# Kernel optimization log

Hardware: AMD Instinct MI355X
Metric: run time of the kernel (lower is better)

## Reference

```python
import jax, jax.numpy as jnp
import numpy as np

DIM = 1024
HEADS = 16
HEAD_DIM = DIM // HEADS
SCALE = HEAD_DIM ** -0.5


def setup_inputs() -> dict:
    key = jax.random.key(0)
    ks = jax.random.split(key, 9)
    B, S, D = 2, 2048, DIM
    std = 1.0 / np.sqrt(D)
    Z = jax.random.normal(ks[0], (B, S, D), dtype=jnp.float32)
    Wq = jax.random.uniform(ks[1], (D, D), jnp.float32, -std, std)
    bq = jax.random.uniform(ks[2], (D,), jnp.float32, -std, std)
    Wk = jax.random.uniform(ks[3], (D, D), jnp.float32, -std, std)
    bk = jax.random.uniform(ks[4], (D,), jnp.float32, -std, std)
    Wv = jax.random.uniform(ks[5], (D, D), jnp.float32, -std, std)
    bv = jax.random.uniform(ks[6], (D,), jnp.float32, -std, std)
    Wo = jax.random.uniform(ks[7], (D, D), jnp.float32, -std, std)
    bo = jax.random.uniform(ks[8], (D,), jnp.float32, -std, std)
    return {"Z": Z, "Wq": Wq, "bq": bq, "Wk": Wk, "bk": bk,
            "Wv": Wv, "bv": bv, "Wo": Wo, "bo": bo}


def reference(Z, Wq, bq, Wk, bk, Wv, bv, Wo, bo):
    B, S, D = Z.shape
    H, Hd = HEADS, HEAD_DIM
    # torch Linear: y = x @ W.T + b
    Q = (Z @ Wq.T + bq).reshape(B, S, H, Hd).transpose(0, 2, 1, 3)  # [B,H,S,Hd]
    K = (Z @ Wk.T + bk).reshape(B, S, H, Hd).transpose(0, 2, 1, 3)
    V = (Z @ Wv.T + bv).reshape(B, S, H, Hd).transpose(0, 2, 1, 3)
    scores = jnp.einsum('bhqd,bhkd->bhqk', Q, K) * SCALE  # [B,H,S,S]
    weights = jax.nn.softmax(scores, axis=-1)
    weights = jnp.nan_to_num(weights, nan=0.0)
    # dropout=0.0 -> identity (eval mode)
    out = jnp.einsum('bhqk,bhkd->bhqd', weights, V)  # [B,H,S,Hd]
    out = out.transpose(0, 2, 1, 3).reshape(B, S, D)
    return out @ Wo.T + bo
```

## Files before the change

kernel.cpp:

```cpp
#include <hip/hip_runtime.h>
#include <hip/hip_bf16.h>
#include <stdint.h>

typedef unsigned short u16;
typedef __bf16 bf16x8 __attribute__((ext_vector_type(8)));
typedef float f32x4 __attribute__((ext_vector_type(4)));
typedef float f32x16 __attribute__((ext_vector_type(16)));

#define D_MODEL 1024
#define SEQ     2048
#define NB      2
#define NH      16
#define HD      64
#define M_TOT   (NB*SEQ)
#define ATT_SCALE 0.125f

__device__ __forceinline__ u16 f2bf(float f) {
  union { __bf16 b; u16 u; } cv; cv.b = (__bf16)f; return cv.u;
}

__device__ __forceinline__ void async_copy16(void* lds_dst, const void* gsrc) {
  __builtin_amdgcn_global_load_lds(
      (const __attribute__((address_space(1))) unsigned int*)gsrc,
      (__attribute__((address_space(3))) unsigned int*)lds_dst, 16, 0, 0);
}

__global__ void cvt_all(const float* __restrict__ Z,  const float* __restrict__ Wq,
                        const float* __restrict__ Wk, const float* __restrict__ Wv,
                        const float* __restrict__ Wo,
                        u16* __restrict__ Zb,  u16* __restrict__ Wqb,
                        u16* __restrict__ Wkb, u16* __restrict__ Wvb,
                        u16* __restrict__ Wob)
{
  int i = blockIdx.x * 256 + threadIdx.x;
  const float* src; u16* dst; int off;
  if (i < (1 << 20)) { src = Z; dst = Zb; off = i; }
  else {
    int j = i - (1 << 20);
    int seg = j >> 18; off = j & ((1 << 18) - 1);
    src = (seg == 0) ? Wq : (seg == 1) ? Wk : (seg == 2) ? Wv : Wo;
    dst = (seg == 0) ? Wqb : (seg == 1) ? Wkb : (seg == 2) ? Wvb : Wob;
  }
  float4 v = reinterpret_cast<const float4*>(src)[off];
  ushort4 o;
  o.x = f2bf(v.x); o.y = f2bf(v.y); o.z = f2bf(v.z); o.w = f2bf(v.w);
  reinterpret_cast<ushort4*>(dst)[off] = o;
}

template<int F32OUT, int TRANSV>
__global__ __launch_bounds__(256, 3)
void gemm_bt(const u16* __restrict__ A,
             const u16* __restrict__ B0, const u16* __restrict__ B1, const u16* __restrict__ B2,
             const float* __restrict__ bias0, const float* __restrict__ bias1, const float* __restrict__ bias2,
             void* __restrict__ C0, void* __restrict__ C1, void* __restrict__ C2,
             float s0, float s1, float s2,
             int M, int N, int K)
{
  (void)M;
  const int z = blockIdx.z;
  const u16* Bt = (z == 0) ? B0 : ((z == 1) ? B1 : B2);
  const float* bias = (z == 0) ? bias0 : ((z == 1) ? bias1 : bias2);
  void* Cout = (z == 0) ? C0 : ((z == 1) ? C1 : C2);
  const float oscl = (z == 0) ? s0 : ((z == 1) ? s1 : s2);

  __shared__ u16 lds_a[2][128*32];
  __shared__ u16 lds_b[2][128*32];

  const int tid = threadIdx.x;
  const int w = tid >> 6, lane = tid & 63;
  const int l15 = lane & 15, lhi = lane >> 4;
  const int m0 = blockIdx.y * 128, n0 = blockIdx.x * 128;
  const int wm = w >> 1, wn = w & 1;

  f32x4 acc[4][4] = {};

  auto stage = [&](int buf, int kt) {
    const int k0 = kt * 32;
    #pragma unroll
    for (int i = 0; i < 2; ++i) {
      const int base = (w*2 + i) * 1024;
      const int pos  = base + (lane << 4);
      const int row  = pos >> 6;
      const int slot = (pos >> 4) & 3;
      const int ss   = slot ^ ((row >> 1) & 3);
      async_copy16((char*)lds_a[buf] + base,
                   (const char*)(A  + (size_t)(m0 + row) * K + k0 + ss*8));
      async_copy16((char*)lds_b[buf] + base,
                   (const char*)(Bt + (size_t)(n0 + row) * K + k0 + ss*8));
    }
  };

  auto compute = [&](int buf) {
    bf16x8 af[4], bf[4];
    #pragma unroll
    for (int mi = 0; mi < 4; ++mi) {
      const int row = wm*64 + mi*16 + l15;
      const int s   = lhi ^ ((row >> 1) & 3);
      af[mi] = *reinterpret_cast<const bf16x8*>((const char*)lds_a[buf] + row*64 + s*16);
    }
    #pragma unroll
    for (int ni = 0; ni < 4; ++ni) {
      const int row = wn*64 + ni*16 + l15;
      const int s   = lhi ^ ((row >> 1) & 3);
      bf[ni] = *reinterpret_cast<const bf16x8*>((const char*)lds_b[buf] + row*64 + s*16);
    }
    #pragma unroll
    for (int mi = 0; mi < 4; ++mi)
      #pragma unroll
      for (int ni = 0; ni < 4; ++ni)
        acc[mi][ni] = __builtin_amdgcn_mfma_f32_16x16x32_bf16(af[mi], bf[ni], acc[mi][ni], 0, 0, 0);
  };

  stage(0, 0);
  __syncthreads();
  const int nk = K >> 5;
  for (int kt = 0; kt < nk; ++kt) {
    if (kt + 1 < nk) stage((kt + 1) & 1, kt + 1);
    compute(kt & 1);
    __syncthreads();
  }

  #pragma unroll
  for (int mi = 0; mi < 4; ++mi) {
    const int rowb = m0 + wm*64 + mi*16 + (lhi << 2);
    #pragma unroll
    for (int ni = 0; ni < 4; ++ni) {
      const int col = n0 + wn*64 + ni*16 + l15;
      const float bb = bias[col];
      if (TRANSV && z == 2) {
        ushort4 o4;
        o4.x = f2bf(acc[mi][ni][0] + bb);
        o4.y = f2bf(acc[mi][ni][1] + bb);
        o4.z = f2bf(acc[mi][ni][2] + bb);
        o4.w = f2bf(acc[mi][ni][3] + bb);
        const int bb2 = rowb >> 11, s = rowb & (SEQ - 1);
        const int hh = col >> 6, dd = col & 63;
        *reinterpret_cast<ushort4*>((u16*)Cout + ((size_t)(bb2*NH + hh)*HD + dd)*SEQ + s) = o4;
      } else {
        #pragma unroll
        for (int r = 0; r < 4; ++r) {
          const float v = (acc[mi][ni][r] + bb) * oscl;
          if (F32OUT)
            reinterpret_cast<float*>(Cout)[(size_t)(rowb + r) * N + col] = v;
          else
            reinterpret_cast<u16*>(Cout)[(size_t)(rowb + r) * N + col] = f2bf(v);
        }
      }
    }
  }
}

__global__ __launch_bounds__(256, 2)
void attn32(const u16* __restrict__ Qb, const u16* __restrict__ Kb,
            const u16* __restrict__ Vt, u16* __restrict__ Ob)
{
  __shared__ u16 vt[2][64*64];

  const int tid = threadIdx.x;
  const int w = tid >> 6, lane = tid & 63;
  const int l31 = lane & 31, hi = lane >> 5;
  const int bh = blockIdx.y, b = bh >> 4, h = bh & 15;
  const int qrow = blockIdx.x * 128 + w * 32 + l31;

  bf16x8 qf[4];
  {
    const u16* qp = Qb + (size_t)(b*SEQ + qrow) * D_MODEL + h*HD + hi*8;
    #pragma unroll
    for (int kc = 0; kc < 4; ++kc)
      qf[kc] = *reinterpret_cast<const bf16x8*>(qp + kc*16);
  }

  const u16* Vtg = Vt + (size_t)bh * HD * SEQ;

  float mrun = -1e30f, lrun = 0.f;
  f32x16 o0 = {}, o1 = {};

  auto stageV = [&](int buf, int kv0) {
    #pragma unroll
    for (int i = 0; i < 2; ++i) {
      const int c = i*256 + tid;
      const int d = c >> 3;
      const int sl = c & 7;
      const int sg = sl ^ (d & 7);
      async_copy16((char*)vt[buf] + (size_t)(i*256 + w*64)*16,
                   (const char*)(Vtg + (size_t)d*SEQ + kv0 + sg*8));
    }
  };

  stageV(0, 0);
  __syncthreads();
  int buf = 0;

  for (int kv0 = 0; kv0 < SEQ; kv0 += 64) {
    if (kv0 + 64 < SEQ) stageV(buf ^ 1, kv0 + 64);

    f32x16 s0 = {}, s1 = {};
    {
      const u16* kp = Kb + (size_t)(b*SEQ + kv0 + l31) * D_MODEL + h*HD + hi*8;
      #pragma unroll
      for (int kc = 0; kc < 4; ++kc) {
        bf16x8 ka = *reinterpret_cast<const bf16x8*>(kp + kc*16);
        s0 = __builtin_amdgcn_mfma_f32_32x32x16_bf16(ka, qf[kc], s0, 0, 0, 0);
      }
      const u16* kp1 = kp + (size_t)32 * D_MODEL;
      #pragma unroll
      for (int kc = 0; kc < 4; ++kc) {
        bf16x8 ka = *reinterpret_cast<const bf16x8*>(kp1 + kc*16);
        s1 = __builtin_amdgcn_mfma_f32_32x32x16_bf16(ka, qf[kc], s1, 0, 0, 0);
      }
    }

    float tmax = s0[0];
    #pragma unroll
    for (int r = 1; r < 16; ++r) tmax = fmaxf(tmax, s0[r]);
    #pragma unroll
    for (int r = 0; r < 16; ++r) tmax = fmaxf(tmax, s1[r]);
    tmax = fmaxf(tmax, __shfl_xor(tmax, 32));
    const float mnew = fmaxf(mrun, tmax);
    float rs = 0.f;
    #pragma unroll
    for (int r = 0; r < 16; ++r) { s0[r] = __expf(s0[r] - mnew); rs += s0[r]; }
    #pragma unroll
    for (int r = 0; r < 16; ++r) { s1[r] = __expf(s1[r] - mnew); rs += s1[r]; }
    rs += __shfl_xor(rs, 32);
    const float a = __expf(mrun - mnew);
    lrun = lrun * a + rs;
    mrun = mnew;
    #pragma unroll
    for (int r = 0; r < 16; ++r) { o0[r] *= a; o1[r] *= a; }

    unsigned pwA[2][8];
    #pragma unroll
    for (int a4 = 0; a4 < 4; ++a4)
      #pragma unroll
      for (int zz = 0; zz < 2; ++zz) {
        pwA[0][a4*2+zz] = (unsigned)f2bf(s0[4*a4+2*zz]) | ((unsigned)f2bf(s0[4*a4+2*zz+1]) << 16);
        pwA[1][a4*2+zz] = (unsigned)f2bf(s1[4*a4+2*zz]) | ((unsigned)f2bf(s1[4*a4+2*zz+1]) << 16);
      }

    const char* vb = (const char*)vt[buf];
    #pragma unroll
    for (int ks = 0; ks < 4; ++ks) {
      const int kb = ks >> 1, sm = ks & 1;
      unsigned keep0 = hi ? pwA[kb][(2*sm+1)*2+0] : pwA[kb][(2*sm)*2+0];
      unsigned keep1 = hi ? pwA[kb][(2*sm+1)*2+1] : pwA[kb][(2*sm)*2+1];
      unsigned send0 = hi ? pwA[kb][(2*sm)*2+0]   : pwA[kb][(2*sm+1)*2+0];
      unsigned send1 = hi ? pwA[kb][(2*sm)*2+1]   : pwA[kb][(2*sm+1)*2+1];
      unsigned recv0 = (unsigned)__shfl_xor((int)send0, 32);
      unsigned recv1 = (unsigned)__shfl_xor((int)send1, 32);
      union { bf16x8 f; unsigned u[4]; } pf;
      pf.u[0] = hi ? recv0 : keep0;
      pf.u[1] = hi ? recv1 : keep1;
      pf.u[2] = hi ? keep0 : recv0;
      pf.u[3] = hi ? keep1 : recv1;

      const int slg = ks*2 + hi;
      const int sw  = slg ^ (l31 & 7);
      bf16x8 va0 = *reinterpret_cast<const bf16x8*>(vb + (size_t)(l31*8 + sw)*16);
      bf16x8 va1 = *reinterpret_cast<const bf16x8*>(vb + (size_t)((l31+32)*8 + sw)*16);

      o0 = __builtin_amdgcn_mfma_f32_32x32x16_bf16(va0, pf.f, o0, 0, 0, 0);
      o1 = __builtin_amdgcn_mfma_f32_32x32x16_bf16(va1, pf.f, o1, 0, 0, 0);
    }

    __syncthreads();
    buf ^= 1;
  }

  const float inv = 1.0f / lrun;
  u16* op = Ob + (size_t)(b*SEQ + qrow) * D_MODEL + h*HD;
  #pragma unroll
  for (int a4 = 0; a4 < 4; ++a4) {
    ushort4 v0, v1;
    v0.x = f2bf(o0[4*a4+0]*inv); v0.y = f2bf(o0[4*a4+1]*inv);
    v0.z = f2bf(o0[4*a4+2]*inv); v0.w = f2bf(o0[4*a4+3]*inv);
    v1.x = f2bf(o1[4*a4+0]*inv); v1.y = f2bf(o1[4*a4+1]*inv);
    v1.z = f2bf(o1[4*a4+2]*inv); v1.w = f2bf(o1[4*a4+3]*inv);
    *reinterpret_cast<ushort4*>(op + 8*a4 + 4*hi)      = v0;
    *reinterpret_cast<ushort4*>(op + 32 + 8*a4 + 4*hi) = v1;
  }
}

extern "C" void kernel_launch(void* const* d_in, const int* in_sizes, int n_in,
                              void* d_out, int out_size, void* d_ws, size_t ws_size,
                              hipStream_t stream)
{
  (void)in_sizes; (void)n_in; (void)out_size;
  const float* Z  = (const float*)d_in[0];
  const float* Wq = (const float*)d_in[1];
  const float* bq = (const float*)d_in[2];
  const float* Wk = (const float*)d_in[3];
  const float* bk = (const float*)d_in[4];
  const float* Wv = (const float*)d_in[5];
  const float* bv = (const float*)d_in[6];
  const float* Wo = (const float*)d_in[7];
  const float* bo = (const float*)d_in[8];
  float* out = (float*)d_out;

  const size_t needed = (size_t)(M_TOT*D_MODEL)*2*5 + (size_t)(D_MODEL*D_MODEL)*2*4;
  if (ws_size < needed) return;

  u16* Zb  = (u16*)d_ws;
  u16* Wqb = Zb  + (size_t)M_TOT*D_MODEL;
  u16* Wkb = Wqb + (size_t)D_MODEL*D_MODEL;
  u16* Wvb = Wkb + (size_t)D_MODEL*D_MODEL;
  u16* Wob = Wvb + (size_t)D_MODEL*D_MODEL;
  u16* Qb  = Wob + (size_t)D_MODEL*D_MODEL;
  u16* Kb  = Qb  + (size_t)M_TOT*D_MODEL;
  u16* Vt  = Kb  + (size_t)M_TOT*D_MODEL;
  u16* Ab  = Vt  + (size_t)M_TOT*D_MODEL;

  cvt_all<<<dim3(8192), 256, 0, stream>>>(Z, Wq, Wk, Wv, Wo, Zb, Wqb, Wkb, Wvb, Wob);

  dim3 gproj(D_MODEL/128, M_TOT/128, 3);
  gemm_bt<0,1><<<gproj, 256, 0, stream>>>(Zb, Wqb, Wkb, Wvb, bq, bk, bv,
                                          (void*)Qb, (void*)Kb, (void*)Vt,
                                          ATT_SCALE, 1.0f, 1.0f,
                                          M_TOT, D_MODEL, D_MODEL);

  dim3 gattn(SEQ/128, NB*NH);
  attn32<<<gattn, 256, 0, stream>>>(Qb, Kb, Vt, Ab);

  dim3 gout(D_MODEL/128, M_TOT/128, 1);
  gemm_bt<1,0><<<gout, 256, 0, stream>>>(Ab, Wob, Wob, Wob, bo, bo, bo,
                                         (void*)out, (void*)out, (void*)out,
                                         1.0f, 1.0f, 1.0f,
                                         M_TOT, D_MODEL, D_MODEL);
}
```

Before: 240.6 us.

## Stage K tiles in LDS, use exp2 softmax with deferred rescale, swap V MFMA

K tiles are now loaded into swizzled LDS double buffers with async copies alongside V, replacing per-lane strided global loads inside the attention loop. The log2(e) factor is folded into the Q scale so softmax uses the hardware exp2, and the running-max rescale is skipped unless some lane's new max exceeds the old one by more than a threshold. In the V projection, the MFMA operands are swapped so the transposed V layout comes straight out of the accumulator. The trade-offs are more LDS per block and unrescaled exponent values that can grow up to 2^8 before a rescale, which costs some numerical headroom.

```diff
diff --git a/kernel.cpp b/kernel.cpp
--- a/kernel.cpp
+++ b/kernel.cpp
@@ -13,10 +13,14 @@
 #define NH      16
 #define HD      64
 #define M_TOT   (NB*SEQ)
-#define ATT_SCALE 0.125f
+#define QSCALE  (0.125f * 1.44269504088896f)
+#define DEFER_THR 8.0f
 
 __device__ __forceinline__ u16 f2bf(float f) {
   union { __bf16 b; u16 u; } cv; cv.b = (__bf16)f; return cv.u;
+}
+__device__ __forceinline__ float exp2_fast(float x) {
+  return __builtin_amdgcn_exp2f(x);
 }
 
 __device__ __forceinline__ void async_copy16(void* lds_dst, const void* gsrc) {
@@ -62,6 +66,7 @@
   const float* bias = (z == 0) ? bias0 : ((z == 1) ? bias1 : bias2);
   void* Cout = (z == 0) ? C0 : ((z == 1) ? C1 : C2);
   const float oscl = (z == 0) ? s0 : ((z == 1) ? s1 : s2);
+  const bool vswap = TRANSV && (z == 2);
 
   __shared__ u16 lds_a[2][128*32];
   __shared__ u16 lds_b[2][128*32];
@@ -104,11 +109,19 @@
       const int s   = lhi ^ ((row >> 1) & 3);
       bf[ni] = *reinterpret_cast<const bf16x8*>((const char*)lds_b[buf] + row*64 + s*16);
     }
-    #pragma unroll
-    for (int mi = 0; mi < 4; ++mi)
-      #pragma unroll
-      for (int ni = 0; ni < 4; ++ni)
-        acc[mi][ni] = __builtin_amdgcn_mfma_f32_16x16x32_bf16(af[mi], bf[ni], acc[mi][ni], 0, 0, 0);
+    if (vswap) {
+      #pragma unroll
+      for (int mi = 0; mi < 4; ++mi)
+        #pragma unroll
+        for (int ni = 0; ni < 4; ++ni)
+          acc[mi][ni] = __builtin_amdgcn_mfma_f32_16x16x32_bf16(bf[ni], af[mi], acc[mi][ni], 0, 0, 0);
+    } else {
+      #pragma unroll
+      for (int mi = 0; mi < 4; ++mi)
+        #pragma unroll
+        for (int ni = 0; ni < 4; ++ni)
+          acc[mi][ni] = __builtin_amdgcn_mfma_f32_16x16x32_bf16(af[mi], bf[ni], acc[mi][ni], 0, 0, 0);
+    }
   };
 
   stage(0, 0);
@@ -120,23 +133,30 @@
     __syncthreads();
   }
 
-  #pragma unroll
-  for (int mi = 0; mi < 4; ++mi) {
-    const int rowb = m0 + wm*64 + mi*16 + (lhi << 2);
-    #pragma unroll
-    for (int ni = 0; ni < 4; ++ni) {
-      const int col = n0 + wn*64 + ni*16 + l15;
-      const float bb = bias[col];
-      if (TRANSV && z == 2) {
-        ushort4 o4;
-        o4.x = f2bf(acc[mi][ni][0] + bb);
-        o4.y = f2bf(acc[mi][ni][1] + bb);
-        o4.z = f2bf(acc[mi][ni][2] + bb);
-        o4.w = f2bf(acc[mi][ni][3] + bb);
-        const int bb2 = rowb >> 11, s = rowb & (SEQ - 1);
-        const int hh = col >> 6, dd = col & 63;
-        *reinterpret_cast<ushort4*>((u16*)Cout + ((size_t)(bb2*NH + hh)*HD + dd)*SEQ + s) = o4;
-      } else {
+  if (vswap) {
+    #pragma unroll
+    for (int mi = 0; mi < 4; ++mi) {
+      const int sglob = m0 + wm*64 + mi*16 + l15;
+      const int b2 = sglob >> 11, s = sglob & (SEQ - 1);
+      #pragma unroll
+      for (int ni = 0; ni < 4; ++ni) {
+        #pragma unroll
+        for (int r = 0; r < 4; ++r) {
+          const int dglob = n0 + wn*64 + ni*16 + (lhi << 2) + r;
+          const int hh = dglob >> 6, dd = dglob & 63;
+          const float v = acc[mi][ni][r] + bias[dglob];
+          reinterpret_cast<u16*>(Cout)[((size_t)(b2*NH + hh)*HD + dd)*SEQ + s] = f2bf(v);
+        }
+      }
+    }
+  } else {
+    #pragma unroll
+    for (int mi = 0; mi < 4; ++mi) {
+      const int rowb = m0 + wm*64 + mi*16 + (lhi << 2);
+      #pragma unroll
+      for (int ni = 0; ni < 4; ++ni) {
+        const int col = n0 + wn*64 + ni*16 + l15;
+        const float bb = bias[col];
         #pragma unroll
         for (int r = 0; r < 4; ++r) {
           const float v = (acc[mi][ni][r] + bb) * oscl;
@@ -155,6 +175,7 @@
             const u16* __restrict__ Vt, u16* __restrict__ Ob)
 {
   __shared__ u16 vt[2][64*64];
+  __shared__ u16 kt[2][64*64];
 
   const int tid = threadIdx.x;
   const int w = tid >> 6, lane = tid & 63;
@@ -171,11 +192,12 @@
   }
 
   const u16* Vtg = Vt + (size_t)bh * HD * SEQ;
+  const u16* Kg  = Kb + (size_t)(b*SEQ) * D_MODEL + h*HD;
 
   float mrun = -1e30f, lrun = 0.f;
   f32x16 o0 = {}, o1 = {};
 
-  auto stageV = [&](int buf, int kv0) {
+  auto stageKV = [&](int buf, int kv0) {
     #pragma unroll
     for (int i = 0; i < 2; ++i) {
       const int c = i*256 + tid;
@@ -185,28 +207,34 @@
       async_copy16((char*)vt[buf] + (size_t)(i*256 + w*64)*16,
                    (const char*)(Vtg + (size_t)d*SEQ + kv0 + sg*8));
     }
+    #pragma unroll
+    for (int i = 0; i < 2; ++i) {
+      const int c = i*256 + tid;
+      const int key = c >> 3;
+      const int sl = c & 7;
+      const int sg = sl ^ (key & 7);
+      async_copy16((char*)kt[buf] + (size_t)(i*256 + w*64)*16,
+                   (const char*)(Kg + (size_t)(kv0 + key)*D_MODEL + sg*8));
+    }
   };
 
-  stageV(0, 0);
+  stageKV(0, 0);
   __syncthreads();
   int buf = 0;
 
   for (int kv0 = 0; kv0 < SEQ; kv0 += 64) {
-    if (kv0 + 64 < SEQ) stageV(buf ^ 1, kv0 + 64);
+    if (kv0 + 64 < SEQ) stageKV(buf ^ 1, kv0 + 64);
 
     f32x16 s0 = {}, s1 = {};
     {
-      const u16* kp = Kb + (size_t)(b*SEQ + kv0 + l31) * D_MODEL + h*HD + hi*8;
+      const char* kbp = (const char*)kt[buf];
       #pragma unroll
       for (int kc = 0; kc < 4; ++kc) {
-        bf16x8 ka = *reinterpret_cast<const bf16x8*>(kp + kc*16);
-        s0 = __builtin_amdgcn_mfma_f32_32x32x16_bf16(ka, qf[kc], s0, 0, 0, 0);
-      }
-      const u16* kp1 = kp + (size_t)32 * D_MODEL;
-      #pragma unroll
-      for (int kc = 0; kc < 4; ++kc) {
-        bf16x8 ka = *reinterpret_cast<const bf16x8*>(kp1 + kc*16);
-        s1 = __builtin_amdgcn_mfma_f32_32x32x16_bf16(ka, qf[kc], s1, 0, 0, 0);
+        const int sw = (kc*2 + hi) ^ (l31 & 7);
+        bf16x8 ka0 = *reinterpret_cast<const bf16x8*>(kbp + (size_t)(l31*8 + sw)*16);
+        s0 = __builtin_amdgcn_mfma_f32_32x32x16_bf16(ka0, qf[kc], s0, 0, 0, 0);
+        bf16x8 ka1 = *reinterpret_cast<const bf16x8*>(kbp + (size_t)((l31+32)*8 + sw)*16);
+        s1 = __builtin_amdgcn_mfma_f32_32x32x16_bf16(ka1, qf[kc], s1, 0, 0, 0);
       }
     }
 
@@ -216,18 +244,21 @@
     #pragma unroll
     for (int r = 0; r < 16; ++r) tmax = fmaxf(tmax, s1[r]);
     tmax = fmaxf(tmax, __shfl_xor(tmax, 32));
-    const float mnew = fmaxf(mrun, tmax);
+    if (!__all(tmax - mrun <= DEFER_THR)) {
+      const float mnew = fmaxf(mrun, tmax);
+      const float a = exp2_fast(mrun - mnew);
+      lrun *= a;
+      #pragma unroll
+      for (int r = 0; r < 16; ++r) { o0[r] *= a; o1[r] *= a; }
+      mrun = mnew;
+    }
     float rs = 0.f;
     #pragma unroll
-    for (int r = 0; r < 16; ++r) { s0[r] = __expf(s0[r] - mnew); rs += s0[r]; }
-    #pragma unroll
-    for (int r = 0; r < 16; ++r) { s1[r] = __expf(s1[r] - mnew); rs += s1[r]; }
+    for (int r = 0; r < 16; ++r) { s0[r] = exp2_fast(s0[r] - mrun); rs += s0[r]; }
+    #pragma unroll
+    for (int r = 0; r < 16; ++r) { s1[r] = exp2_fast(s1[r] - mrun); rs += s1[r]; }
     rs += __shfl_xor(rs, 32);
-    const float a = __expf(mrun - mnew);
-    lrun = lrun * a + rs;
-    mrun = mnew;
-    #pragma unroll
-    for (int r = 0; r < 16; ++r) { o0[r] *= a; o1[r] *= a; }
+    lrun += rs;
 
     unsigned pwA[2][8];
     #pragma unroll
@@ -315,7 +346,7 @@
   dim3 gproj(D_MODEL/128, M_TOT/128, 3);
   gemm_bt<0,1><<<gproj, 256, 0, stream>>>(Zb, Wqb, Wkb, Wvb, bq, bk, bv,
                                           (void*)Qb, (void*)Kb, (void*)Vt,
-                                          ATT_SCALE, 1.0f, 1.0f,
+                                          QSCALE, 1.0f, 1.0f,
                                           M_TOT, D_MODEL, D_MODEL);
 
   dim3 gattn(SEQ/128, NB*NH);
```

After: 239.0 us. No clear change (-0.7%).
